# Kernel optimization log

Measured on AMD Instinct MI355X. Metric: run time of the kernel, lower is better.

## Reference

```python
import jax, jax.numpy as jnp
import numpy as np

N_QUBITS = 12
N_LAYERS = 6
BATCH = 256
INPUT_DIM = 256
OUT_DIM = 64
PI = float(np.pi)


def _ry_mat(a):
    # a: scalar or (B,) real angle -> (...,2,2) complex64 RY matrix
    c, s = jnp.cos(a * 0.5), jnp.sin(a * 0.5)
    return jnp.stack([jnp.stack([c, -s], -1), jnp.stack([s, c], -1)], -2).astype(jnp.complex64)


def _rz_mat(a):
    # diag(e^{-i a/2}, e^{+i a/2})
    em = jnp.exp(-0.5j * a.astype(jnp.complex64))
    ep = jnp.exp(0.5j * a.astype(jnp.complex64))
    z = jnp.zeros_like(em)
    return jnp.stack([jnp.stack([em, z], -1), jnp.stack([z, ep], -1)], -2)


def _apply_1q(state, U, w):
    # shared (2,2) gate on wire w; state: (B, 2, ..., 2)
    s = jnp.moveaxis(state, w + 1, -1)
    s = jnp.einsum('ij,b...j->b...i', U, s)
    return jnp.moveaxis(s, -1, w + 1)


def _apply_1q_batched(state, U, w):
    # per-sample (B,2,2) gate on wire w
    s = jnp.moveaxis(state, w + 1, -1)
    s = jnp.einsum('bij,b...j->b...i', U, s)
    return jnp.moveaxis(s, -1, w + 1)


def _cnot(state, c, t):
    s0 = jnp.take(state, 0, axis=c + 1)
    s1 = jnp.take(state, 1, axis=c + 1)
    t_ax = t + 1 if t < c else t  # target axis index after removing control axis
    s1 = jnp.flip(s1, axis=t_ax)
    return jnp.stack([s0, s1], axis=c + 1)


def _cz(state, c, t):
    idx = [slice(None)] * (N_QUBITS + 1)
    idx[c + 1] = 1
    idx[t + 1] = 1
    return state.at[tuple(idx)].multiply(-1.0)


def _run_circuit(xq, q_weights):
    # xq: (B, n_qubits) in [-1,1]; forward passes xq*pi, circuit multiplies by pi again
    B = xq.shape[0]
    enc = xq * (PI * PI)
    state = jnp.zeros((B, 2 ** N_QUBITS), jnp.complex64).at[:, 0].set(1.0)
    state = state.reshape((B,) + (2,) * N_QUBITS)
    for i in range(N_QUBITS):
        state = _apply_1q_batched(state, _ry_mat(enc[:, i]), i)
    w = q_weights.reshape(N_LAYERS, N_QUBITS, 3)
    for layer in range(N_LAYERS):
        for i in range(N_QUBITS):
            # PennyLane order: RZ(w0) then RY(w1) then RZ(w2) -> U = RZ2 @ RY1 @ RZ0
            U = _rz_mat(w[layer, i, 2]) @ _ry_mat(w[layer, i, 1]) @ _rz_mat(w[layer, i, 0])
            state = _apply_1q(state, U, i)
        for i in range(N_QUBITS):
            state = _cnot(state, i, (i + 1) % N_QUBITS)
        if layer % 2 == 0 and layer < N_LAYERS - 1:
            for i in range(N_QUBITS):
                state = _apply_1q_batched(state, _ry_mat(enc[:, i] * 0.5), i)
        if layer % 2 == 1:
            for i in range(0, N_QUBITS - 2, 2):
                state = _cz(state, i, i + 2)
    # PauliZ expectation on wires 0,1,2
    p = (state.real ** 2 + state.imag ** 2).reshape(B, 2, 2, 2, -1).sum(-1)  # (B,2,2,2)
    z0 = (p[:, 0] - p[:, 1]).sum((-1, -2))
    z1 = (p[:, :, 0] - p[:, :, 1]).sum((-1, -2))
    z2 = (p[:, :, :, 0] - p[:, :, :, 1]).sum((-1, -2))
    return jnp.stack([z0, z1, z2], -1)  # (B, 3) float32


def _layernorm(h, g, b, eps=1e-5):
    mu = h.mean(-1, keepdims=True)
    var = ((h - mu) ** 2).mean(-1, keepdims=True)
    return (h - mu) * jax.lax.rsqrt(var + eps) * g + b


def _forward(x, W1, b1, g_ln, b_ln, W2, b2, W3, b3, q_weights, W4, b4, W5, b5):
    gelu = lambda t: jax.nn.gelu(t, approximate=False)
    h = gelu(x @ W1.T + b1)
    h = _layernorm(h, g_ln, b_ln)
    h = gelu(h @ W2.T + b2)
    xq = jnp.tanh(h @ W3.T + b3)  # (B, n_qubits)
    q = _run_circuit(xq, q_weights)  # (B, 3)
    return gelu(q @ W4.T + b4) @ W5.T + b5  # (B, OUT_DIM)


def setup_inputs() -> dict:
    key = jax.random.key(0)
    ks = jax.random.split(key, 8)
    rn = lambda k, shape, s=0.05: (jax.random.normal(k, shape) * s).astype(jnp.float32)
    return {
        'x': jax.random.normal(ks[0], (BATCH, INPUT_DIM), jnp.float32),
        'W1': rn(ks[1], (128, INPUT_DIM)), 'b1': jnp.zeros(128, jnp.float32),
        'g_ln': jnp.ones(128, jnp.float32), 'b_ln': jnp.zeros(128, jnp.float32),
        'W2': rn(ks[2], (64, 128)), 'b2': jnp.zeros(64, jnp.float32),
        'W3': rn(ks[3], (N_QUBITS, 64)), 'b3': jnp.zeros(N_QUBITS, jnp.float32),
        'q_weights': (jax.random.normal(ks[4], (N_LAYERS * N_QUBITS * 3,)) * 0.1).astype(jnp.float32),
        'W4': rn(ks[5], (32, 3)), 'b4': jnp.zeros(32, jnp.float32),
        'W5': rn(ks[6], (OUT_DIM, 32)), 'b5': jnp.zeros(OUT_DIM, jnp.float32),
    }


def reference(x, W1, b1, g_ln, b_ln, W2, b2, W3, b3, q_weights, W4, b4, W5, b5):
    return _forward(x, W1, b1, g_ln, b_ln, W2, b2, W3, b3, q_weights, W4, b4, W5, b5)
```

## Files before the change

kernel.cpp:

```cpp
#include <hip/hip_runtime.h>
#include <math.h>

#define NQ   12
#define NL   6
#define BATCH 256
#define NT   512
#define PI2  9.869604401089358f

typedef float v2f __attribute__((ext_vector_type(2)));

__device__ __forceinline__ float geluf(float x) {
    return 0.5f * x * (1.0f + erff(x * 0.70710678118654752f));
}

__device__ __forceinline__ int Pad(int x) { return x + (x >> 4) + (x >> 8); }

__device__ __forceinline__ int gmap(int j) {
    return ((j ^ (j >> 1)) & 0x3FF)
         | ((((j >> 10) ^ (j >> 11) ^ j) & 1) << 10)
         | ((((j >> 11) ^ j) & 1) << 11);
}

__device__ __forceinline__ int sigma(int x) {
    return ((x & 0x1E) << 6) | ((x & 0x780) >> 6)
         | ((x & 0x41) << 5) | ((x & 0x820) >> 5);
}

template<int CTRL>
__device__ __forceinline__ v2f dppv(v2f v) {
    int x = __builtin_amdgcn_update_dpp(0, __float_as_int(v.x), CTRL, 0xF, 0xF, true);
    int y = __builtin_amdgcn_update_dpp(0, __float_as_int(v.y), CTRL, 0xF, 0xF, true);
    v2f r; r.x = __int_as_float(x); r.y = __int_as_float(y); return r;
}

__global__ __launch_bounds__(NT)
void qpu_kernel(const float* __restrict__ x,   const float* __restrict__ W1, const float* __restrict__ b1,
                const float* __restrict__ g_ln, const float* __restrict__ b_ln,
                const float* __restrict__ W2,  const float* __restrict__ b2,
                const float* __restrict__ W3,  const float* __restrict__ b3,
                const float* __restrict__ qw,  const float* __restrict__ W4, const float* __restrict__ b4,
                const float* __restrict__ W5,  const float* __restrict__ b5,
                float* __restrict__ out)
{
    __shared__ float2 bufA[4368];
    __shared__ float2 bufB[4368];
    __shared__ float  Umr[5 * 12 * 8];
    __shared__ float4 L0c[12];
    __shared__ float  xs[256];
    __shared__ float  pr[1280];
    __shared__ float  h1n[128];
    __shared__ float  h2s[64];
    __shared__ float  xqs[NQ];
    __shared__ float  musd[2];
    __shared__ float  qv[3];
    __shared__ float  h4s[32];
    __shared__ float  zred[8][3];

    const int t = threadIdx.x;
    const int b = blockIdx.x;

    if (t < 256) xs[t] = x[b * 256 + t];
    __syncthreads();

    {
        const int o = t >> 2, part = t & 3;
        const float4* w  = (const float4*)(W1 + o * 256) + part * 16;
        const float*  xp = xs + part * 64;
        float a0 = 0.f, a1 = 0.f, a2 = 0.f, a3 = 0.f;
        #pragma unroll
        for (int k = 0; k < 16; k++) {
            float4 wv = w[k];
            a0 = fmaf(wv.x, xp[4 * k + 0], a0);
            a1 = fmaf(wv.y, xp[4 * k + 1], a1);
            a2 = fmaf(wv.z, xp[4 * k + 2], a2);
            a3 = fmaf(wv.w, xp[4 * k + 3], a3);
        }
        pr[o * 5 + part] = (a0 + a1) + (a2 + a3);
    }
    __syncthreads();
    if (t < 128) {
        float s = pr[t * 5 + 0] + pr[t * 5 + 1] + pr[t * 5 + 2] + pr[t * 5 + 3];
        h1n[t] = geluf(s + b1[t]);
    }
    __syncthreads();

    if (t < 64) {
        float v0 = h1n[t], v1 = h1n[t + 64];
        float s1 = v0 + v1;
        float s2 = fmaf(v0, v0, v1 * v1);
        #pragma unroll
        for (int off = 32; off > 0; off >>= 1) {
            s1 += __shfl_down(s1, off);
            s2 += __shfl_down(s2, off);
        }
        if (t == 0) {
            float mu  = s1 * (1.f / 128.f);
            float var = s2 * (1.f / 128.f) - mu * mu;
            musd[0] = mu;
            musd[1] = rsqrtf(var + 1e-5f);
        }
    }
    __syncthreads();
    if (t < 128) h1n[t] = (h1n[t] - musd[0]) * musd[1] * g_ln[t] + b_ln[t];
    __syncthreads();

    {
        const int o = t >> 3, part = t & 7;
        const float4* w  = (const float4*)(W2 + o * 128) + part * 4;
        const float*  hp = h1n + part * 16;
        float a0 = 0.f, a1 = 0.f, a2 = 0.f, a3 = 0.f;
        #pragma unroll
        for (int k = 0; k < 4; k++) {
            float4 wv = w[k];
            a0 = fmaf(wv.x, hp[4 * k + 0], a0);
            a1 = fmaf(wv.y, hp[4 * k + 1], a1);
            a2 = fmaf(wv.z, hp[4 * k + 2], a2);
            a3 = fmaf(wv.w, hp[4 * k + 3], a3);
        }
        pr[o * 9 + part] = (a0 + a1) + (a2 + a3);
    }
    __syncthreads();
    if (t < 64) {
        float s = 0.f;
        #pragma unroll
        for (int k = 0; k < 8; k++) s += pr[t * 9 + k];
        h2s[t] = geluf(s + b2[t]);
    }
    __syncthreads();

    if (t < 96) {
        const int o = t >> 3, part = t & 7;
        const float4* w  = (const float4*)(W3 + o * 64) + part * 2;
        const float*  hp = h2s + part * 8;
        float4 w0 = w[0], w1 = w[1];
        float s = 0.f;
        s = fmaf(w0.x, hp[0], s); s = fmaf(w0.y, hp[1], s);
        s = fmaf(w0.z, hp[2], s); s = fmaf(w0.w, hp[3], s);
        s = fmaf(w1.x, hp[4], s); s = fmaf(w1.y, hp[5], s);
        s = fmaf(w1.z, hp[6], s); s = fmaf(w1.w, hp[7], s);
        pr[o * 9 + part] = s;
    }
    __syncthreads();
    if (t < NQ) {
        float s = 0.f;
        #pragma unroll
        for (int k = 0; k < 8; k++) s += pr[t * 9 + k];
        xqs[t] = tanhf(s + b3[t]);
    }
    __syncthreads();

    if (t < NL * NQ) {
        const int l = t / NQ;
        const int i = t % NQ;
        float a  = qw[t * 3 + 0];
        float bb = qw[t * 3 + 1];
        float c  = qw[t * 3 + 2];
        float sb, cb;   sincosf(0.5f * bb, &sb, &cb);
        float apc = 0.5f * (a + c), amc = 0.5f * (a - c);
        float sapc, capc; sincosf(apc, &sapc, &capc);
        float samc, camc; sincosf(amc, &samc, &camc);
        float u00x =  cb * capc, u00y = -cb * sapc;
        float u01x = -sb * camc, u01y = -sb * samc;
        float u10x =  sb * camc, u10y = -sb * samc;
        float u11x =  cb * capc, u11y =  cb * sapc;

        float theta = 0.f;
        bool merge = false;
        if (l == 0)      { theta = xqs[i] * PI2;        merge = true; }
        else if (l & 1)  { theta = xqs[i] * PI2 * 0.5f; merge = true; }
        if (merge) {
            float sy, cy; sincosf(0.5f * theta, &sy, &cy);
            float m00x = u00x * cy + u01x * sy,  m00y = u00y * cy + u01y * sy;
            float m01x = -u00x * sy + u01x * cy, m01y = -u00y * sy + u01y * cy;
            float m10x = u10x * cy + u11x * sy,  m10y = u10y * cy + u11y * sy;
            float m11x = -u10x * sy + u11x * cy, m11y = -u10y * sy + u11y * cy;
            u00x = m00x; u00y = m00y; u01x = m01x; u01y = m01y;
            u10x = m10x; u10y = m10y; u11x = m11x; u11y = m11y;
        }
        if (l == 0) {
            L0c[i] = make_float4(u00x, u00y, u10x, u10y);
        } else {
            float* d = &Umr[((l - 1) * 12 + i) * 8];
            if (i == 11 || i == 6) {
                d[0] = u00x; d[1] = u10x; d[2] = u00y; d[3] = u10y;
                d[4] = u01x; d[5] = u11x; d[6] = u01y; d[7] = u11y;
            } else if (i == 10 || i == 9 || i == 4 || i == 3) {
                d[0] = u00x; d[1] = u00y; d[2] = u01x; d[3] = u01y;
                d[4] = u10x; d[5] = u10y; d[6] = u11x; d[7] = u11y;
            } else {
                d[0] = u00x; d[1] = u00y; d[2] = u01x; d[3] = u01y;
                d[4] = u11x; d[5] = u11y; d[6] = u10x; d[7] = u10y;
            }
        }
    }
    __syncthreads();

    const int PwA = 8 * t + (t >> 1) + (t >> 5);
    const int s8t = sigma(8 * t);
    const int Ps  = Pad(s8t);
    const int SD[8] = {0, 34, 136, 170, 273, 307, 409, 443};
    const int g8t = gmap(8 * t);
    const int GMm[8] = {0, 0xC01, 3, 0xC02, 6, 0xC07, 5, 0xC04};
    int   qm[8];
    float czm[8];
    #pragma unroll
    for (int m = 0; m < 8; m++) {
        qm[m] = Pad(g8t ^ GMm[m]);
        const int j = 8 * t + m;
        czm[m] = (__popc(j & (j << 2) & 0xAA8) & 1) ? -1.f : 1.f;
    }
    const bool t0 = t & 1, t1 = t & 2, t3 = t & 8;

    v2f R[4], I[4];
    {
        float cr, ci;
        {
            const float4 f = L0c[8];
            const bool bit = (g8t >> 3) & 1;
            cr = bit ? f.z : f.x; ci = bit ? f.w : f.y;
        }
        #pragma unroll
        for (int k = 4; k <= 9; k++) {
            const float4 f = L0c[11 - k];
            const bool bit = (g8t >> k) & 1;
            const float fr = bit ? f.z : f.x, fi = bit ? f.w : f.y;
            const float nr = cr * fr - ci * fi;
            const float ni = cr * fi + ci * fr;
            cr = nr; ci = ni;
        }
        #pragma unroll
        for (int m = 0; m < 8; m++) {
            const int g = g8t ^ GMm[m];
            float rr = cr, ii = ci;
            const int KB[5] = {0, 1, 2, 10, 11};
            #pragma unroll
            for (int q = 0; q < 5; q++) {
                const int k = KB[q];
                const float4 f = L0c[11 - k];
                const bool bit = (g >> k) & 1;
                const float fr = bit ? f.z : f.x, fi = bit ? f.w : f.y;
                const float nr = rr * fr - ii * fi;
                const float ni = rr * fi + ii * fr;
                rr = nr; ii = ni;
            }
            if (m & 1) { R[m >> 1].y = rr; I[m >> 1].y = ii; }
            else       { R[m >> 1].x = rr; I[m >> 1].x = ii; }
        }
    }

    #define GATE_IP(BASE) do {                                                \
        const float4 A  = *(const float4*)(BASE);                             \
        const float4 Bq = *(const float4*)((BASE) + 4);                       \
        v2f CAr, CAi, CBr, CBi;                                               \
        CAr.x = A.x;  CAr.y = A.y;  CAi.x = A.z;  CAi.y = A.w;                \
        CBr.x = Bq.x; CBr.y = Bq.y; CBi.x = Bq.z; CBi.y = Bq.w;               \
        _Pragma("unroll")                                                     \
        for (int k = 0; k < 4; k++) {                                         \
            v2f rxx, ryy, ixx, iyy;                                           \
            rxx.x = R[k].x; rxx.y = R[k].x; ryy.x = R[k].y; ryy.y = R[k].y;   \
            ixx.x = I[k].x; ixx.y = I[k].x; iyy.x = I[k].y; iyy.y = I[k].y;   \
            v2f nR = CAr * rxx - CAi * ixx + CBr * ryy - CBi * iyy;           \
            v2f nI = CAi * rxx + CAr * ixx + CBi * ryy + CBr * iyy;           \
            R[k] = nR; I[k] = nI;                                             \
        } } while (0)

    #define GATE_CP_PAIR(c0, c1, A0, B0) do {                                 \
        v2f Ra = R[A0], Ia = I[A0], Rb = R[B0], Ib = I[B0];                   \
        R[A0] = c0.x * Ra - c0.y * Ia + c0.z * Rb - c0.w * Ib;                \
        I[A0] = c0.y * Ra + c0.x * Ia + c0.w * Rb + c0.z * Ib;                \
        R[B0] = c1.x * Ra - c1.y * Ia + c1.z * Rb - c1.w * Ib;                \
        I[B0] = c1.y * Ra + c1.x * Ia + c1.w * Rb + c1.z * Ib;                \
        } while (0)

    #define GATE_CP(BASE, A0, B0, A1, B1) do {                                \
        const float4 c0 = *(const float4*)(BASE);                             \
        const float4 c1 = *(const float4*)((BASE) + 4);                       \
        GATE_CP_PAIR(c0, c1, A0, B0);                                         \
        GATE_CP_PAIR(c0, c1, A1, B1);                                         \
        } while (0)

    #define GATE_DPP(BASE, SEL, CTRL) do {                                    \
        const float4 c = *(const float4*)((BASE) + ((SEL) ? 4 : 0));          \
        _Pragma("unroll")                                                     \
        for (int k = 0; k < 4; k++) {                                         \
            v2f vR = dppv<CTRL>(R[k]);                                        \
            v2f vI = dppv<CTRL>(I[k]);                                        \
            v2f nR = c.x * R[k] - c.y * I[k] + c.z * vR - c.w * vI;           \
            v2f nI = c.y * R[k] + c.x * I[k] + c.w * vR + c.z * vI;           \
            R[k] = nR; I[k] = nI;                                             \
        } } while (0)

    #pragma unroll 1
    for (int l = 1; l < NL; l++) {
        const float* UL = &Umr[(l - 1) * 96];

        GATE_IP(UL + 11 * 8);
        GATE_CP(UL + 10 * 8, 0, 1, 2, 3);
        GATE_CP(UL +  9 * 8, 0, 2, 1, 3);
        GATE_DPP(UL + 8 * 8, t0, 0xB1);
        GATE_DPP(UL + 7 * 8, t1, 0x4E);
        GATE_DPP(UL + 5 * 8, t3, 0x128);

        {
            float2* w = &bufA[PwA];
            w[0] = make_float2(R[0].x, I[0].x);
            w[1] = make_float2(R[0].y, I[0].y);
            w[2] = make_float2(R[1].x, I[1].x);
            w[3] = make_float2(R[1].y, I[1].y);
            w[4] = make_float2(R[2].x, I[2].x);
            w[5] = make_float2(R[2].y, I[2].y);
            w[6] = make_float2(R[3].x, I[3].x);
            w[7] = make_float2(R[3].y, I[3].y);
            __syncthreads();
            #pragma unroll
            for (int m = 0; m < 8; m++) {
                const float2 v = bufA[Ps + SD[m]];
                if (m & 1) { R[m >> 1].y = v.x; I[m >> 1].y = v.y; }
                else       { R[m >> 1].x = v.x; I[m >> 1].x = v.y; }
            }
        }

        GATE_IP(UL + 6 * 8);
        GATE_CP(UL + 4 * 8, 0, 1, 2, 3);
        GATE_CP(UL + 3 * 8, 0, 2, 1, 3);
        GATE_DPP(UL + 2 * 8, t0, 0xB1);
        GATE_DPP(UL + 1 * 8, t1, 0x4E);
        GATE_DPP(UL + 0 * 8, t3, 0x128);

        if (l < NL - 1) {
            #pragma unroll
            for (int m = 0; m < 8; m++) {
                float2 v;
                if (m & 1) { v.x = R[m >> 1].y; v.y = I[m >> 1].y; }
                else       { v.x = R[m >> 1].x; v.y = I[m >> 1].x; }
                bufB[Ps + SD[m]] = v;
            }
            __syncthreads();
            const bool czl = (l == 1) || (l == 3);
            #pragma unroll
            for (int m = 0; m < 8; m++) {
                float2 v = bufB[qm[m]];
                if (czl) { v.x *= czm[m]; v.y *= czm[m]; }
                if (m & 1) { R[m >> 1].y = v.x; I[m >> 1].y = v.y; }
                else       { R[m >> 1].x = v.x; I[m >> 1].x = v.y; }
            }
        }
    }
    #undef GATE_IP
    #undef GATE_CP
    #undef GATE_CP_PAIR
    #undef GATE_DPP

    float p[8];
    p[0] = R[0].x * R[0].x + I[0].x * I[0].x;
    p[1] = R[0].y * R[0].y + I[0].y * I[0].y;
    p[2] = R[1].x * R[1].x + I[1].x * I[1].x;
    p[3] = R[1].y * R[1].y + I[1].y * I[1].y;
    p[4] = R[2].x * R[2].x + I[2].x * I[2].x;
    p[5] = R[2].y * R[2].y + I[2].y * I[2].y;
    p[6] = R[3].x * R[3].x + I[3].x * I[3].x;
    p[7] = R[3].y * R[3].y + I[3].y * I[3].y;
    float alt = (p[0] - p[1] - p[2] + p[3]) - (p[4] - p[5] - p[6] + p[7]);
    float tot = (p[0] + p[1] + p[2] + p[3]) + (p[4] + p[5] + p[6] + p[7]);
    float z0 = (__popc(t & 0x1F7) & 1) ? -alt : alt;
    float z1 = (__popc(t & 0x00A) & 1) ? -tot : tot;
    float z2 = (__popc(t & 0x00B) & 1) ? -tot : tot;

    #pragma unroll
    for (int off = 32; off > 0; off >>= 1) {
        z0 += __shfl_down(z0, off);
        z1 += __shfl_down(z1, off);
        z2 += __shfl_down(z2, off);
    }
    if ((t & 63) == 0) {
        zred[t >> 6][0] = z0;
        zred[t >> 6][1] = z1;
        zred[t >> 6][2] = z2;
    }
    __syncthreads();
    if (t == 0) {
        float q0 = 0.f, q1 = 0.f, q2 = 0.f;
        #pragma unroll
        for (int w = 0; w < 8; w++) {
            q0 += zred[w][0]; q1 += zred[w][1]; q2 += zred[w][2];
        }
        qv[0] = q0; qv[1] = q1; qv[2] = q2;
    }
    __syncthreads();

    if (t < 32) {
        float h = b4[t];
        h = fmaf(qv[0], W4[t * 3 + 0], h);
        h = fmaf(qv[1], W4[t * 3 + 1], h);
        h = fmaf(qv[2], W4[t * 3 + 2], h);
        h4s[t] = geluf(h);
    }
    __syncthreads();
    if (t < 64) {
        float acc = b5[t];
        #pragma unroll
        for (int h = 0; h < 32; h++) acc = fmaf(h4s[h], W5[t * 32 + h], acc);
        out[b * 64 + t] = acc;
    }
}

extern "C" void kernel_launch(void* const* d_in, const int* in_sizes, int n_in,
                              void* d_out, int out_size, void* d_ws, size_t ws_size,
                              hipStream_t stream) {
    (void)in_sizes; (void)n_in; (void)d_ws; (void)ws_size; (void)out_size;
    const float* x    = (const float*)d_in[0];
    const float* W1   = (const float*)d_in[1];
    const float* b1   = (const float*)d_in[2];
    const float* g_ln = (const float*)d_in[3];
    const float* b_ln = (const float*)d_in[4];
    const float* W2   = (const float*)d_in[5];
    const float* b2   = (const float*)d_in[6];
    const float* W3   = (const float*)d_in[7];
    const float* b3   = (const float*)d_in[8];
    const float* qw   = (const float*)d_in[9];
    const float* W4   = (const float*)d_in[10];
    const float* b4   = (const float*)d_in[11];
    const float* W5   = (const float*)d_in[12];
    const float* b5   = (const float*)d_in[13];
    float* out = (float*)d_out;

    qpu_kernel<<<BATCH, NT, 0, stream>>>(x, W1, b1, g_ln, b_ln, W2, b2,
                                         W3, b3, qw, W4, b4, W5, b5, out);
}
```

Measured before the change: 103.0 us.

## Use persistent blocks with an atomic work counter and weight prefetch

The kernel now launches a fixed grid of 384 blocks. Each block loops, taking the next sample index from a global atomic counter that is reset with a memset in the workspace, and keeps going until all 256 samples are done. Before the loop, each thread touches W2, W3, W5 and qw, multiplied by zero, to warm the caches early. This adds a memset launch and per-sample atomic traffic, and with only 256 samples the extra 128 blocks mostly just fetch a counter and exit.

```diff
diff --git a/kernel.cpp b/kernel.cpp
--- a/kernel.cpp
+++ b/kernel.cpp
@@ -5,6 +5,7 @@
 #define NL   6
 #define BATCH 256
 #define NT   512
+#define GRID 384
 #define PI2  9.869604401089358f
 
 typedef float v2f __attribute__((ext_vector_type(2)));
@@ -40,7 +41,7 @@
                 const float* __restrict__ W3,  const float* __restrict__ b3,
                 const float* __restrict__ qw,  const float* __restrict__ W4, const float* __restrict__ b4,
                 const float* __restrict__ W5,  const float* __restrict__ b5,
-                float* __restrict__ out)
+                float* __restrict__ out, unsigned* __restrict__ counter)
 {
     __shared__ float2 bufA[4368];
     __shared__ float2 bufB[4368];
@@ -55,145 +56,18 @@
     __shared__ float  qv[3];
     __shared__ float  h4s[32];
     __shared__ float  zred[8][3];
+    __shared__ unsigned s_samp;
 
     const int t = threadIdx.x;
-    const int b = blockIdx.x;
-
-    if (t < 256) xs[t] = x[b * 256 + t];
-    __syncthreads();
-
+
+    float pf;
     {
-        const int o = t >> 2, part = t & 3;
-        const float4* w  = (const float4*)(W1 + o * 256) + part * 16;
-        const float*  xp = xs + part * 64;
-        float a0 = 0.f, a1 = 0.f, a2 = 0.f, a3 = 0.f;
-        #pragma unroll
-        for (int k = 0; k < 16; k++) {
-            float4 wv = w[k];
-            a0 = fmaf(wv.x, xp[4 * k + 0], a0);
-            a1 = fmaf(wv.y, xp[4 * k + 1], a1);
-            a2 = fmaf(wv.z, xp[4 * k + 2], a2);
-            a3 = fmaf(wv.w, xp[4 * k + 3], a3);
-        }
-        pr[o * 5 + part] = (a0 + a1) + (a2 + a3);
+        float p0 = W2[(t * 16) & 8191];
+        float p1 = W3[t & 511];
+        float p2 = W5[(t * 4) & 2047];
+        float p3 = qw[t & 127];
+        pf = ((p0 + p1) + (p2 + p3)) * 0.0f;
     }
-    __syncthreads();
-    if (t < 128) {
-        float s = pr[t * 5 + 0] + pr[t * 5 + 1] + pr[t * 5 + 2] + pr[t * 5 + 3];
-        h1n[t] = geluf(s + b1[t]);
-    }
-    __syncthreads();
-
-    if (t < 64) {
-        float v0 = h1n[t], v1 = h1n[t + 64];
-        float s1 = v0 + v1;
-        float s2 = fmaf(v0, v0, v1 * v1);
-        #pragma unroll
-        for (int off = 32; off > 0; off >>= 1) {
-            s1 += __shfl_down(s1, off);
-            s2 += __shfl_down(s2, off);
-        }
-        if (t == 0) {
-            float mu  = s1 * (1.f / 128.f);
-            float var = s2 * (1.f / 128.f) - mu * mu;
-            musd[0] = mu;
-            musd[1] = rsqrtf(var + 1e-5f);
-        }
-    }
-    __syncthreads();
-    if (t < 128) h1n[t] = (h1n[t] - musd[0]) * musd[1] * g_ln[t] + b_ln[t];
-    __syncthreads();
-
-    {
-        const int o = t >> 3, part = t & 7;
-        const float4* w  = (const float4*)(W2 + o * 128) + part * 4;
-        const float*  hp = h1n + part * 16;
-        float a0 = 0.f, a1 = 0.f, a2 = 0.f, a3 = 0.f;
-        #pragma unroll
-        for (int k = 0; k < 4; k++) {
-            float4 wv = w[k];
-            a0 = fmaf(wv.x, hp[4 * k + 0], a0);
-            a1 = fmaf(wv.y, hp[4 * k + 1], a1);
-            a2 = fmaf(wv.z, hp[4 * k + 2], a2);
-            a3 = fmaf(wv.w, hp[4 * k + 3], a3);
-        }
-        pr[o * 9 + part] = (a0 + a1) + (a2 + a3);
-    }
-    __syncthreads();
-    if (t < 64) {
-        float s = 0.f;
-        #pragma unroll
-        for (int k = 0; k < 8; k++) s += pr[t * 9 + k];
-        h2s[t] = geluf(s + b2[t]);
-    }
-    __syncthreads();
-
-    if (t < 96) {
-        const int o = t >> 3, part = t & 7;
-        const float4* w  = (const float4*)(W3 + o * 64) + part * 2;
-        const float*  hp = h2s + part * 8;
-        float4 w0 = w[0], w1 = w[1];
-        float s = 0.f;
-        s = fmaf(w0.x, hp[0], s); s = fmaf(w0.y, hp[1], s);
-        s = fmaf(w0.z, hp[2], s); s = fmaf(w0.w, hp[3], s);
-        s = fmaf(w1.x, hp[4], s); s = fmaf(w1.y, hp[5], s);
-        s = fmaf(w1.z, hp[6], s); s = fmaf(w1.w, hp[7], s);
-        pr[o * 9 + part] = s;
-    }
-    __syncthreads();
-    if (t < NQ) {
-        float s = 0.f;
-        #pragma unroll
-        for (int k = 0; k < 8; k++) s += pr[t * 9 + k];
-        xqs[t] = tanhf(s + b3[t]);
-    }
-    __syncthreads();
-
-    if (t < NL * NQ) {
-        const int l = t / NQ;
-        const int i = t % NQ;
-        float a  = qw[t * 3 + 0];
-        float bb = qw[t * 3 + 1];
-        float c  = qw[t * 3 + 2];
-        float sb, cb;   sincosf(0.5f * bb, &sb, &cb);
-        float apc = 0.5f * (a + c), amc = 0.5f * (a - c);
-        float sapc, capc; sincosf(apc, &sapc, &capc);
-        float samc, camc; sincosf(amc, &samc, &camc);
-        float u00x =  cb * capc, u00y = -cb * sapc;
-        float u01x = -sb * camc, u01y = -sb * samc;
-        float u10x =  sb * camc, u10y = -sb * samc;
-        float u11x =  cb * capc, u11y =  cb * sapc;
-
-        float theta = 0.f;
-        bool merge = false;
-        if (l == 0)      { theta = xqs[i] * PI2;        merge = true; }
-        else if (l & 1)  { theta = xqs[i] * PI2 * 0.5f; merge = true; }
-        if (merge) {
-            float sy, cy; sincosf(0.5f * theta, &sy, &cy);
-            float m00x = u00x * cy + u01x * sy,  m00y = u00y * cy + u01y * sy;
-            float m01x = -u00x * sy + u01x * cy, m01y = -u00y * sy + u01y * cy;
-            float m10x = u10x * cy + u11x * sy,  m10y = u10y * cy + u11y * sy;
-            float m11x = -u10x * sy + u11x * cy, m11y = -u10y * sy + u11y * cy;
-            u00x = m00x; u00y = m00y; u01x = m01x; u01y = m01y;
-            u10x = m10x; u10y = m10y; u11x = m11x; u11y = m11y;
-        }
-        if (l == 0) {
-            L0c[i] = make_float4(u00x, u00y, u10x, u10y);
-        } else {
-            float* d = &Umr[((l - 1) * 12 + i) * 8];
-            if (i == 11 || i == 6) {
-                d[0] = u00x; d[1] = u10x; d[2] = u00y; d[3] = u10y;
-                d[4] = u01x; d[5] = u11x; d[6] = u01y; d[7] = u11y;
-            } else if (i == 10 || i == 9 || i == 4 || i == 3) {
-                d[0] = u00x; d[1] = u00y; d[2] = u01x; d[3] = u01y;
-                d[4] = u10x; d[5] = u10y; d[6] = u11x; d[7] = u11y;
-            } else {
-                d[0] = u00x; d[1] = u00y; d[2] = u01x; d[3] = u01y;
-                d[4] = u11x; d[5] = u11y; d[6] = u10x; d[7] = u10y;
-            }
-        }
-    }
-    __syncthreads();
 
     const int PwA = 8 * t + (t >> 1) + (t >> 5);
     const int s8t = sigma(8 * t);
@@ -211,203 +85,347 @@
     }
     const bool t0 = t & 1, t1 = t & 2, t3 = t & 8;
 
-    v2f R[4], I[4];
-    {
-        float cr, ci;
+    for (;;) {
+        __syncthreads();
+        if (t == 0) s_samp = atomicAdd(counter, 1u);
+        __syncthreads();
+        const int b = (int)s_samp;
+        if (b >= BATCH) break;
+
+        if (t < 256) xs[t] = x[b * 256 + t];
+        __syncthreads();
+
         {
-            const float4 f = L0c[8];
-            const bool bit = (g8t >> 3) & 1;
-            cr = bit ? f.z : f.x; ci = bit ? f.w : f.y;
-        }
+            const int o = t >> 2, part = t & 3;
+            const float4* w  = (const float4*)(W1 + o * 256) + part * 16;
+            const float*  xp = xs + part * 64;
+            float a0 = 0.f, a1 = 0.f, a2 = 0.f, a3 = 0.f;
+            #pragma unroll
+            for (int k = 0; k < 16; k++) {
+                float4 wv = w[k];
+                a0 = fmaf(wv.x, xp[4 * k + 0], a0);
+                a1 = fmaf(wv.y, xp[4 * k + 1], a1);
+                a2 = fmaf(wv.z, xp[4 * k + 2], a2);
+                a3 = fmaf(wv.w, xp[4 * k + 3], a3);
+            }
+            pr[o * 5 + part] = (a0 + a1) + (a2 + a3) + pf;
+        }
+        __syncthreads();
+        if (t < 128) {
+            float s = pr[t * 5 + 0] + pr[t * 5 + 1] + pr[t * 5 + 2] + pr[t * 5 + 3];
+            h1n[t] = geluf(s + b1[t]);
+        }
+        __syncthreads();
+
+        if (t < 64) {
+            float v0 = h1n[t], v1 = h1n[t + 64];
+            float s1 = v0 + v1;
+            float s2 = fmaf(v0, v0, v1 * v1);
+            #pragma unroll
+            for (int off = 32; off > 0; off >>= 1) {
+                s1 += __shfl_down(s1, off);
+                s2 += __shfl_down(s2, off);
+            }
+            if (t == 0) {
+                float mu  = s1 * (1.f / 128.f);
+                float var = s2 * (1.f / 128.f) - mu * mu;
+                musd[0] = mu;
+                musd[1] = rsqrtf(var + 1e-5f);
+            }
+        }
+        __syncthreads();
+        if (t < 128) h1n[t] = (h1n[t] - musd[0]) * musd[1] * g_ln[t] + b_ln[t];
+        __syncthreads();
+
+        {
+            const int o = t >> 3, part = t & 7;
+            const float4* w  = (const float4*)(W2 + o * 128) + part * 4;
+            const float*  hp = h1n + part * 16;
+            float a0 = 0.f, a1 = 0.f, a2 = 0.f, a3 = 0.f;
+            #pragma unroll
+            for (int k = 0; k < 4; k++) {
+                float4 wv = w[k];
+                a0 = fmaf(wv.x, hp[4 * k + 0], a0);
+                a1 = fmaf(wv.y, hp[4 * k + 1], a1);
+                a2 = fmaf(wv.z, hp[4 * k + 2], a2);
+                a3 = fmaf(wv.w, hp[4 * k + 3], a3);
+            }
+            pr[o * 9 + part] = (a0 + a1) + (a2 + a3);
+        }
+        __syncthreads();
+        if (t < 64) {
+            float s = 0.f;
+            #pragma unroll
+            for (int k = 0; k < 8; k++) s += pr[t * 9 + k];
+            h2s[t] = geluf(s + b2[t]);
+        }
+        __syncthreads();
+
+        if (t < 96) {
+            const int o = t >> 3, part = t & 7;
+            const float4* w  = (const float4*)(W3 + o * 64) + part * 2;
+            const float*  hp = h2s + part * 8;
+            float4 w0 = w[0], w1 = w[1];
+            float s = 0.f;
+            s = fmaf(w0.x, hp[0], s); s = fmaf(w0.y, hp[1], s);
+            s = fmaf(w0.z, hp[2], s); s = fmaf(w0.w, hp[3], s);
+            s = fmaf(w1.x, hp[4], s); s = fmaf(w1.y, hp[5], s);
+            s = fmaf(w1.z, hp[6], s); s = fmaf(w1.w, hp[7], s);
+            pr[o * 9 + part] = s;
+        }
+        __syncthreads();
+        if (t < NQ) {
+            float s = 0.f;
+            #pragma unroll
+            for (int k = 0; k < 8; k++) s += pr[t * 9 + k];
+            xqs[t] = tanhf(s + b3[t]);
+        }
+        __syncthreads();
+
+        if (t < NL * NQ) {
+            const int l = t / NQ;
+            const int i = t % NQ;
+            float a  = qw[t * 3 + 0];
+            float bb = qw[t * 3 + 1];
+            float c  = qw[t * 3 + 2];
+            float sb, cb;   sincosf(0.5f * bb, &sb, &cb);
+            float apc = 0.5f * (a + c), amc = 0.5f * (a - c);
+            float sapc, capc; sincosf(apc, &sapc, &capc);
+            float samc, camc; sincosf(amc, &samc, &camc);
+            float u00x =  cb * capc, u00y = -cb * sapc;
+            float u01x = -sb * camc, u01y = -sb * samc;
+            float u10x =  sb * camc, u10y = -sb * samc;
+            float u11x =  cb * capc, u11y =  cb * sapc;
+
+            float theta = 0.f;
+            bool merge = false;
+            if (l == 0)      { theta = xqs[i] * PI2;        merge = true; }
+            else if (l & 1)  { theta = xqs[i] * PI2 * 0.5f; merge = true; }
+            if (merge) {
+                float sy, cy; sincosf(0.5f * theta, &sy, &cy);
+                float m00x = u00x * cy + u01x * sy,  m00y = u00y * cy + u01y * sy;
+                float m01x = -u00x * sy + u01x * cy, m01y = -u00y * sy + u01y * cy;
+                float m10x = u10x * cy + u11x * sy,  m10y = u10y * cy + u11y * sy;
+                float m11x = -u10x * sy + u11x * cy, m11y = -u10y * sy + u11y * cy;
+                u00x = m00x; u00y = m00y; u01x = m01x; u01y = m01y;
+                u10x = m10x; u10y = m10y; u11x = m11x; u11y = m11y;
+            }
+            if (l == 0) {
+                L0c[i] = make_float4(u00x, u00y, u10x, u10y);
+            } else {
+                float* d = &Umr[((l - 1) * 12 + i) * 8];
+                if (i == 11 || i == 6) {
+                    d[0] = u00x; d[1] = u10x; d[2] = u00y; d[3] = u10y;
+                    d[4] = u01x; d[5] = u11x; d[6] = u01y; d[7] = u11y;
+                } else if (i == 10 || i == 9 || i == 4 || i == 3) {
+                    d[0] = u00x; d[1] = u00y; d[2] = u01x; d[3] = u01y;
+                    d[4] = u10x; d[5] = u10y; d[6] = u11x; d[7] = u11y;
+                } else {
+                    d[0] = u00x; d[1] = u00y; d[2] = u01x; d[3] = u01y;
+                    d[4] = u11x; d[5] = u11y; d[6] = u10x; d[7] = u10y;
+                }
+            }
+        }
+        __syncthreads();
+
+        v2f R[4], I[4];
+        {
+            float cr, ci;
+            {
+                const float4 f = L0c[8];
+                const bool bit = (g8t >> 3) & 1;
+                cr = bit ? f.z : f.x; ci = bit ? f.w : f.y;
+            }
+            #pragma unroll
+            for (int k = 4; k <= 9; k++) {
+                const float4 f = L0c[11 - k];
+                const bool bit = (g8t >> k) & 1;
+                const float fr = bit ? f.z : f.x, fi = bit ? f.w : f.y;
+                const float nr = cr * fr - ci * fi;
+                const float ni = cr * fi + ci * fr;
+                cr = nr; ci = ni;
+            }
+            #pragma unroll
+            for (int m = 0; m < 8; m++) {
+                const int g = g8t ^ GMm[m];
+                float rr = cr, ii = ci;
+                const int KB[5] = {0, 1, 2, 10, 11};
+                #pragma unroll
+                for (int q = 0; q < 5; q++) {
+                    const int k = KB[q];
+                    const float4 f = L0c[11 - k];
+                    const bool bit = (g >> k) & 1;
+                    const float fr = bit ? f.z : f.x, fi = bit ? f.w : f.y;
+                    const float nr = rr * fr - ii * fi;
+                    const float ni = rr * fi + ii * fr;
+                    rr = nr; ii = ni;
+                }
+                if (m & 1) { R[m >> 1].y = rr; I[m >> 1].y = ii; }
+                else       { R[m >> 1].x = rr; I[m >> 1].x = ii; }
+            }
+        }
+
+        #define GATE_IP(BASE) do {                                                \
+            const float4 A  = *(const float4*)(BASE);                             \
+            const float4 Bq = *(const float4*)((BASE) + 4);                       \
+            v2f CAr, CAi, CBr, CBi;                                               \
+            CAr.x = A.x;  CAr.y = A.y;  CAi.x = A.z;  CAi.y = A.w;                \
+            CBr.x = Bq.x; CBr.y = Bq.y; CBi.x = Bq.z; CBi.y = Bq.w;               \
+            _Pragma("unroll")                                                     \
+            for (int k = 0; k < 4; k++) {                                         \
+                v2f rxx, ryy, ixx, iyy;                                           \
+                rxx.x = R[k].x; rxx.y = R[k].x; ryy.x = R[k].y; ryy.y = R[k].y;   \
+                ixx.x = I[k].x; ixx.y = I[k].x; iyy.x = I[k].y; iyy.y = I[k].y;   \
+                v2f nR = CAr * rxx - CAi * ixx + CBr * ryy - CBi * iyy;           \
+                v2f nI = CAi * rxx + CAr * ixx + CBi * ryy + CBr * iyy;           \
+                R[k] = nR; I[k] = nI;                                             \
+            } } while (0)
+
+        #define GATE_CP_PAIR(c0, c1, A0, B0) do {                                 \
+            v2f Ra = R[A0], Ia = I[A0], Rb = R[B0], Ib = I[B0];                   \
+            R[A0] = c0.x * Ra - c0.y * Ia + c0.z * Rb - c0.w * Ib;                \
+            I[A0] = c0.y * Ra + c0.x * Ia + c0.w * Rb + c0.z * Ib;                \
+            R[B0] = c1.x * Ra - c1.y * Ia + c1.z * Rb - c1.w * Ib;                \
+            I[B0] = c1.y * Ra + c1.x * Ia + c1.w * Rb + c1.z * Ib;                \
+            } while (0)
+
+        #define GATE_CP(BASE, A0, B0, A1, B1) do {                                \
+            const float4 c0 = *(const float4*)(BASE);                             \
+            const float4 c1 = *(const float4*)((BASE) + 4);                       \
+            GATE_CP_PAIR(c0, c1, A0, B0);                                         \
+            GATE_CP_PAIR(c0, c1, A1, B1);                                         \
+            } while (0)
+
+        #define GATE_DPP(BASE, SEL, CTRL) do {                                    \
+            const float4 c = *(const float4*)((BASE) + ((SEL) ? 4 : 0));          \
+            _Pragma("unroll")                                                     \
+            for (int k = 0; k < 4; k++) {                                         \
+                v2f vR = dppv<CTRL>(R[k]);                                        \
+                v2f vI = dppv<CTRL>(I[k]);                                        \
+                v2f nR = c.x * R[k] - c.y * I[k] + c.z * vR - c.w * vI;           \
+                v2f nI = c.y * R[k] + c.x * I[k] + c.w * vR + c.z * vI;           \
+                R[k] = nR; I[k] = nI;                                             \
+            } } while (0)
+
+        #pragma unroll 1
+        for (int l = 1; l < NL; l++) {
+            const float* UL = &Umr[(l - 1) * 96];
+
+            GATE_IP(UL + 11 * 8);
+            GATE_CP(UL + 10 * 8, 0, 1, 2, 3);
+            GATE_CP(UL +  9 * 8, 0, 2, 1, 3);
+            GATE_DPP(UL + 8 * 8, t0, 0xB1);
+            GATE_DPP(UL + 7 * 8, t1, 0x4E);
+            GATE_DPP(UL + 5 * 8, t3, 0x128);
+
+            {
+                float2* w = &bufA[PwA];
+                w[0] = make_float2(R[0].x, I[0].x);
+                w[1] = make_float2(R[0].y, I[0].y);
+                w[2] = make_float2(R[1].x, I[1].x);
+                w[3] = make_float2(R[1].y, I[1].y);
+                w[4] = make_float2(R[2].x, I[2].x);
+                w[5] = make_float2(R[2].y, I[2].y);
+                w[6] = make_float2(R[3].x, I[3].x);
+                w[7] = make_float2(R[3].y, I[3].y);
+                __syncthreads();
+                #pragma unroll
+                for (int m = 0; m < 8; m++) {
+                    const float2 v = bufA[Ps + SD[m]];
+                    if (m & 1) { R[m >> 1].y = v.x; I[m >> 1].y = v.y; }
+                    else       { R[m >> 1].x = v.x; I[m >> 1].x = v.y; }
+                }
+            }
+
+            GATE_IP(UL + 6 * 8);
+            GATE_CP(UL + 4 * 8, 0, 1, 2, 3);
+            GATE_CP(UL + 3 * 8, 0, 2, 1, 3);
+            GATE_DPP(UL + 2 * 8, t0, 0xB1);
+            GATE_DPP(UL + 1 * 8, t1, 0x4E);
+            GATE_DPP(UL + 0 * 8, t3, 0x128);
+
+            if (l < NL - 1) {
+                #pragma unroll
+                for (int m = 0; m < 8; m++) {
+                    float2 v;
+                    if (m & 1) { v.x = R[m >> 1].y; v.y = I[m >> 1].y; }
+                    else       { v.x = R[m >> 1].x; v.y = I[m >> 1].x; }
+                    bufB[Ps + SD[m]] = v;
+                }
+                __syncthreads();
+                const bool czl = (l == 1) || (l == 3);
+                #pragma unroll
+                for (int m = 0; m < 8; m++) {
+                    float2 v = bufB[qm[m]];
+                    if (czl) { v.x *= czm[m]; v.y *= czm[m]; }
+                    if (m & 1) { R[m >> 1].y = v.x; I[m >> 1].y = v.y; }
+                    else       { R[m >> 1].x = v.x; I[m >> 1].x = v.y; }
+                }
+            }
+        }
+        #undef GATE_IP
+        #undef GATE_CP
+        #undef GATE_CP_PAIR
+        #undef GATE_DPP
+
+        float p[8];
+        p[0] = R[0].x * R[0].x + I[0].x * I[0].x;
+        p[1] = R[0].y * R[0].y + I[0].y * I[0].y;
+        p[2] = R[1].x * R[1].x + I[1].x * I[1].x;
+        p[3] = R[1].y * R[1].y + I[1].y * I[1].y;
+        p[4] = R[2].x * R[2].x + I[2].x * I[2].x;
+        p[5] = R[2].y * R[2].y + I[2].y * I[2].y;
+        p[6] = R[3].x * R[3].x + I[3].x * I[3].x;
+        p[7] = R[3].y * R[3].y + I[3].y * I[3].y;
+        float alt = (p[0] - p[1] - p[2] + p[3]) - (p[4] - p[5] - p[6] + p[7]);
+        float tot = (p[0] + p[1] + p[2] + p[3]) + (p[4] + p[5] + p[6] + p[7]);
+        float z0 = (__popc(t & 0x1F7) & 1) ? -alt : alt;
+        float z1 = (__popc(t & 0x00A) & 1) ? -tot : tot;
+        float z2 = (__popc(t & 0x00B) & 1) ? -tot : tot;
+
         #pragma unroll
-        for (int k = 4; k <= 9; k++) {
-            const float4 f = L0c[11 - k];
-            const bool bit = (g8t >> k) & 1;
-            const float fr = bit ? f.z : f.x, fi = bit ? f.w : f.y;
-            const float nr = cr * fr - ci * fi;
-            const float ni = cr * fi + ci * fr;
-            cr = nr; ci = ni;
-        }
-        #pragma unroll
-        for (int m = 0; m < 8; m++) {
-            const int g = g8t ^ GMm[m];
-            float rr = cr, ii = ci;
-            const int KB[5] = {0, 1, 2, 10, 11};
-            #pragma unroll
-            for (int q = 0; q < 5; q++) {
-                const int k = KB[q];
-                const float4 f = L0c[11 - k];
-                const bool bit = (g >> k) & 1;
-                const float fr = bit ? f.z : f.x, fi = bit ? f.w : f.y;
-                const float nr = rr * fr - ii * fi;
-                const float ni = rr * fi + ii * fr;
-                rr = nr; ii = ni;
-            }
-            if (m & 1) { R[m >> 1].y = rr; I[m >> 1].y = ii; }
-            else       { R[m >> 1].x = rr; I[m >> 1].x = ii; }
-        }
-    }
-
-    #define GATE_IP(BASE) do {                                                \
-        const float4 A  = *(const float4*)(BASE);                             \
-        const float4 Bq = *(const float4*)((BASE) + 4);                       \
-        v2f CAr, CAi, CBr, CBi;                                               \
-        CAr.x = A.x;  CAr.y = A.y;  CAi.x = A.z;  CAi.y = A.w;                \
-        CBr.x = Bq.x; CBr.y = Bq.y; CBi.x = Bq.z; CBi.y = Bq.w;               \
-        _Pragma("unroll")                                                     \
-        for (int k = 0; k < 4; k++) {                                         \
-            v2f rxx, ryy, ixx, iyy;                                           \
-            rxx.x = R[k].x; rxx.y = R[k].x; ryy.x = R[k].y; ryy.y = R[k].y;   \
-            ixx.x = I[k].x; ixx.y = I[k].x; iyy.x = I[k].y; iyy.y = I[k].y;   \
-            v2f nR = CAr * rxx - CAi * ixx + CBr * ryy - CBi * iyy;           \
-            v2f nI = CAi * rxx + CAr * ixx + CBi * ryy + CBr * iyy;           \
-            R[k] = nR; I[k] = nI;                                             \
-        } } while (0)
-
-    #define GATE_CP_PAIR(c0, c1, A0, B0) do {                                 \
-        v2f Ra = R[A0], Ia = I[A0], Rb = R[B0], Ib = I[B0];                   \
-        R[A0] = c0.x * Ra - c0.y * Ia + c0.z * Rb - c0.w * Ib;                \
-        I[A0] = c0.y * Ra + c0.x * Ia + c0.w * Rb + c0.z * Ib;                \
-        R[B0] = c1.x * Ra - c1.y * Ia + c1.z * Rb - c1.w * Ib;                \
-        I[B0] = c1.y * Ra + c1.x * Ia + c1.w * Rb + c1.z * Ib;                \
-        } while (0)
-
-    #define GATE_CP(BASE, A0, B0, A1, B1) do {                                \
-        const float4 c0 = *(const float4*)(BASE);                             \
-        const float4 c1 = *(const float4*)((BASE) + 4);                       \
-        GATE_CP_PAIR(c0, c1, A0, B0);                                         \
-        GATE_CP_PAIR(c0, c1, A1, B1);                                         \
-        } while (0)
-
-    #define GATE_DPP(BASE, SEL, CTRL) do {                                    \
-        const float4 c = *(const float4*)((BASE) + ((SEL) ? 4 : 0));          \
-        _Pragma("unroll")                                                     \
-        for (int k = 0; k < 4; k++) {                                         \
-            v2f vR = dppv<CTRL>(R[k]);                                        \
-            v2f vI = dppv<CTRL>(I[k]);                                        \
-            v2f nR = c.x * R[k] - c.y * I[k] + c.z * vR - c.w * vI;           \
-            v2f nI = c.y * R[k] + c.x * I[k] + c.w * vR + c.z * vI;           \
-            R[k] = nR; I[k] = nI;                                             \
-        } } while (0)
-
-    #pragma unroll 1
-    for (int l = 1; l < NL; l++) {
-        const float* UL = &Umr[(l - 1) * 96];
-
-        GATE_IP(UL + 11 * 8);
-        GATE_CP(UL + 10 * 8, 0, 1, 2, 3);
-        GATE_CP(UL +  9 * 8, 0, 2, 1, 3);
-        GATE_DPP(UL + 8 * 8, t0, 0xB1);
-        GATE_DPP(UL + 7 * 8, t1, 0x4E);
-        GATE_DPP(UL + 5 * 8, t3, 0x128);
-
-        {
-            float2* w = &bufA[PwA];
-            w[0] = make_float2(R[0].x, I[0].x);
-            w[1] = make_float2(R[0].y, I[0].y);
-            w[2] = make_float2(R[1].x, I[1].x);
-            w[3] = make_float2(R[1].y, I[1].y);
-            w[4] = make_float2(R[2].x, I[2].x);
-            w[5] = make_float2(R[2].y, I[2].y);
-            w[6] = make_float2(R[3].x, I[3].x);
-            w[7] = make_float2(R[3].y, I[3].y);
-            __syncthreads();
-            #pragma unroll
-            for (int m = 0; m < 8; m++) {
-                const float2 v = bufA[Ps + SD[m]];
-                if (m & 1) { R[m >> 1].y = v.x; I[m >> 1].y = v.y; }
-                else       { R[m >> 1].x = v.x; I[m >> 1].x = v.y; }
-            }
-        }
-
-        GATE_IP(UL + 6 * 8);
-        GATE_CP(UL + 4 * 8, 0, 1, 2, 3);
-        GATE_CP(UL + 3 * 8, 0, 2, 1, 3);
-        GATE_DPP(UL + 2 * 8, t0, 0xB1);
-        GATE_DPP(UL + 1 * 8, t1, 0x4E);
-        GATE_DPP(UL + 0 * 8, t3, 0x128);
-
-        if (l < NL - 1) {
-            #pragma unroll
-            for (int m = 0; m < 8; m++) {
-                float2 v;
-                if (m & 1) { v.x = R[m >> 1].y; v.y = I[m >> 1].y; }
-                else       { v.x = R[m >> 1].x; v.y = I[m >> 1].x; }
-                bufB[Ps + SD[m]] = v;
-            }
-            __syncthreads();
-            const bool czl = (l == 1) || (l == 3);
-            #pragma unroll
-            for (int m = 0; m < 8; m++) {
-                float2 v = bufB[qm[m]];
-                if (czl) { v.x *= czm[m]; v.y *= czm[m]; }
-                if (m & 1) { R[m >> 1].y = v.x; I[m >> 1].y = v.y; }
-                else       { R[m >> 1].x = v.x; I[m >> 1].x = v.y; }
-            }
-        }
-    }
-    #undef GATE_IP
-    #undef GATE_CP
-    #undef GATE_CP_PAIR
-    #undef GATE_DPP
-
-    float p[8];
-    p[0] = R[0].x * R[0].x + I[0].x * I[0].x;
-    p[1] = R[0].y * R[0].y + I[0].y * I[0].y;
-    p[2] = R[1].x * R[1].x + I[1].x * I[1].x;
-    p[3] = R[1].y * R[1].y + I[1].y * I[1].y;
-    p[4] = R[2].x * R[2].x + I[2].x * I[2].x;
-    p[5] = R[2].y * R[2].y + I[2].y * I[2].y;
-    p[6] = R[3].x * R[3].x + I[3].x * I[3].x;
-    p[7] = R[3].y * R[3].y + I[3].y * I[3].y;
-    float alt = (p[0] - p[1] - p[2] + p[3]) - (p[4] - p[5] - p[6] + p[7]);
-    float tot = (p[0] + p[1] + p[2] + p[3]) + (p[4] + p[5] + p[6] + p[7]);
-    float z0 = (__popc(t & 0x1F7) & 1) ? -alt : alt;
-    float z1 = (__popc(t & 0x00A) & 1) ? -tot : tot;
-    float z2 = (__popc(t & 0x00B) & 1) ? -tot : tot;
-
-    #pragma unroll
-    for (int off = 32; off > 0; off >>= 1) {
-        z0 += __shfl_down(z0, off);
-        z1 += __shfl_down(z1, off);
-        z2 += __shfl_down(z2, off);
-    }
-    if ((t & 63) == 0) {
-        zred[t >> 6][0] = z0;
-        zred[t >> 6][1] = z1;
-        zred[t >> 6][2] = z2;
-    }
-    __syncthreads();
-    if (t == 0) {
-        float q0 = 0.f, q1 = 0.f, q2 = 0.f;
-        #pragma unroll
-        for (int w = 0; w < 8; w++) {
-            q0 += zred[w][0]; q1 += zred[w][1]; q2 += zred[w][2];
-        }
-        qv[0] = q0; qv[1] = q1; qv[2] = q2;
-    }
-    __syncthreads();
-
-    if (t < 32) {
-        float h = b4[t];
-        h = fmaf(qv[0], W4[t * 3 + 0], h);
-        h = fmaf(qv[1], W4[t * 3 + 1], h);
-        h = fmaf(qv[2], W4[t * 3 + 2], h);
-        h4s[t] = geluf(h);
-    }
-    __syncthreads();
-    if (t < 64) {
-        float acc = b5[t];
-        #pragma unroll
-        for (int h = 0; h < 32; h++) acc = fmaf(h4s[h], W5[t * 32 + h], acc);
-        out[b * 64 + t] = acc;
+        for (int off = 32; off > 0; off >>= 1) {
+            z0 += __shfl_down(z0, off);
+            z1 += __shfl_down(z1, off);
+            z2 += __shfl_down(z2, off);
+        }
+        if ((t & 63) == 0) {
+            zred[t >> 6][0] = z0;
+            zred[t >> 6][1] = z1;
+            zred[t >> 6][2] = z2;
+        }
+        __syncthreads();
+        if (t == 0) {
+            float q0 = 0.f, q1 = 0.f, q2 = 0.f;
+            #pragma unroll
+            for (int w = 0; w < 8; w++) {
+                q0 += zred[w][0]; q1 += zred[w][1]; q2 += zred[w][2];
+            }
+            qv[0] = q0; qv[1] = q1; qv[2] = q2;
+        }
+        __syncthreads();
+
+        if (t < 32) {
+            float h = b4[t];
+            h = fmaf(qv[0], W4[t * 3 + 0], h);
+            h = fmaf(qv[1], W4[t * 3 + 1], h);
+            h = fmaf(qv[2], W4[t * 3 + 2], h);
+            h4s[t] = geluf(h);
+        }
+        __syncthreads();
+        if (t < 64) {
+            float acc = b5[t];
+            #pragma unroll
+            for (int h = 0; h < 32; h++) acc = fmaf(h4s[h], W5[t * 32 + h], acc);
+            out[b * 64 + t] = acc;
+        }
     }
 }
 
 extern "C" void kernel_launch(void* const* d_in, const int* in_sizes, int n_in,
                               void* d_out, int out_size, void* d_ws, size_t ws_size,
                               hipStream_t stream) {
-    (void)in_sizes; (void)n_in; (void)d_ws; (void)ws_size; (void)out_size;
+    (void)in_sizes; (void)n_in; (void)ws_size; (void)out_size;
     const float* x    = (const float*)d_in[0];
     const float* W1   = (const float*)d_in[1];
     const float* b1   = (const float*)d_in[2];
@@ -424,6 +442,8 @@
     const float* b5   = (const float*)d_in[13];
     float* out = (float*)d_out;
 
-    qpu_kernel<<<BATCH, NT, 0, stream>>>(x, W1, b1, g_ln, b_ln, W2, b2,
-                                         W3, b3, qw, W4, b4, W5, b5, out);
-}
+    hipMemsetAsync(d_ws, 0, 64, stream);
+    qpu_kernel<<<GRID, NT, 0, stream>>>(x, W1, b1, g_ln, b_ln, W2, b2,
+                                        W3, b3, qw, W4, b4, W5, b5, out,
+                                        (unsigned*)d_ws);
+}
```

Measured after the change: 110.3 us. 7.1% more time.
